# Kernel tuning notes

Hardware: AMD Instinct MI355X
Metric: run time of the kernel (lower is better)

## Reference

```python
import jax, jax.numpy as jnp
import numpy as np

B, N, D = 8, 8192, 64          # batch, input points, point feature dim
NPOINT, NSAMPLE = 1024, 16     # FPS samples S, KNN neighbors K
WN, OUT = 16, 128              # weightnet out channels, output channels
CIN = 3 + D                    # concat(xyz_norm, point feats) = linear in_channel
NEG_SLOPE = 0.1


def setup_inputs() -> dict:
    key = jax.random.key(0)
    ks = jax.random.split(key, 8)
    rn = lambda k, shp, s: jax.random.normal(k, shp, jnp.float32) * s
    return {
        "xyz": rn(ks[0], (B, 3, N), 1.0),
        "points": rn(ks[1], (B, D, N), 1.0),
        "w1": rn(ks[2], (3, 8), 0.5), "b1": jnp.zeros((8,), jnp.float32),
        "w2": rn(ks[3], (8, 8), 0.35), "b2": jnp.zeros((8,), jnp.float32),
        "w3": rn(ks[4], (8, WN), 0.35), "b3": jnp.zeros((WN,), jnp.float32),
        "lin_w": rn(ks[5], (WN * CIN, OUT), 0.03),
        "lin_b": jnp.zeros((OUT,), jnp.float32),
    }


def _fps(xyz):
    """Furthest point sampling. xyz: [B,N,3] -> idx [B,NPOINT] int32."""
    def step(carry, _):
        dist, farthest = carry  # [B,N], [B]
        centroid = jnp.take_along_axis(xyz, farthest[:, None, None], axis=1)  # [B,1,3]
        d = jnp.sum((xyz - centroid) ** 2, axis=-1)  # [B,N]
        dist = jnp.minimum(dist, d)
        return (dist, jnp.argmax(dist, axis=-1).astype(jnp.int32)), farthest
    init = (jnp.full((xyz.shape[0], xyz.shape[1]), 1e10, xyz.dtype),
            jnp.zeros((xyz.shape[0],), jnp.int32))
    _, idxs = jax.lax.scan(step, init, None, length=NPOINT)
    return idxs.T  # [B, NPOINT]


def reference(xyz, points, w1, b1, w2, b2, w3, b3, lin_w, lin_b):
    xyz_t = xyz.transpose(0, 2, 1)       # [B,N,3]
    pts_t = points.transpose(0, 2, 1)    # [B,N,D]

    fps_idx = _fps(xyz_t)                                   # [B,S]
    bidx = jnp.arange(B)[:, None]
    new_xyz = xyz_t[bidx, fps_idx]                          # [B,S,3]

    # KNN: squared distances (same ordering as euclidean cdist)
    sqr = jnp.sum((new_xyz[:, :, None, :] - xyz_t[:, None, :, :]) ** 2, axis=-1)  # [B,S,N]
    _, knn = jax.lax.top_k(-sqr, NSAMPLE)                   # [B,S,K]

    b3i = jnp.arange(B)[:, None, None]
    g_xyz = xyz_t[b3i, knn]                                 # [B,S,K,3]
    g_xyz_norm = g_xyz - new_xyz[:, :, None, :]             # [B,S,K,3]
    g_pts = pts_t[b3i, knn]                                 # [B,S,K,D]
    feat = jnp.concatenate([g_xyz_norm, g_pts], axis=-1)    # [B,S,K,3+D]

    # WeightNet: 1x1 convs == per-neighbor MLP on xyz offsets
    h = jax.nn.relu(g_xyz_norm @ w1 + b1)
    h = jax.nn.relu(h @ w2 + b2)
    wts = jax.nn.relu(h @ w3 + b3)                          # [B,S,K,WN]

    # weighted aggregation over K, then flatten [C, WN]
    agg = jnp.einsum('bskc,bskw->bscw', feat, wts).reshape(B, NPOINT, CIN * WN)
    out = agg @ lin_w + lin_b                               # [B,S,OUT]
    out = jnp.where(out > 0, out, NEG_SLOPE * out)          # LeakyReLU(0.1)

    return new_xyz.transpose(0, 2, 1), out.transpose(0, 2, 1), fps_idx
```

## Files before the change

### kernel.cpp

```cpp
#include <hip/hip_runtime.h>
#include <hip/hip_bf16.h>

#define NPTS   8192
#define NBATCH 8
#define S      1024
#define K      16
#define D      64
#define CIN    67
#define WN     16
#define OUTC   128

#define OUT_MAIN 24576
#define OUT_FPS  1073152

#define T_FPS   0
#define T_TP    8
#define T_WK    1032
#define NBLK    1544

#define SCOPE __HIP_MEMORY_SCOPE_AGENT

typedef float v2f __attribute__((ext_vector_type(2)));

struct Ctrl {
  int ticket;
  int pad0[31];
  int tp_done[8];
  int pad1[24];
  int prog[8];
};

__device__ __forceinline__ unsigned long long aload64(const unsigned long long* p) {
  return __hip_atomic_load(p, __ATOMIC_RELAXED, SCOPE);
}
__device__ __forceinline__ void astore64(unsigned long long* p, unsigned long long v) {
  __hip_atomic_store(p, v, __ATOMIC_RELAXED, SCOPE);
}

__device__ __forceinline__ void barrier_lgkm() {
  asm volatile("s_waitcnt lgkmcnt(0)\n\ts_barrier" ::: "memory");
}

template <int CTRL, int RM>
__device__ __forceinline__ unsigned long long dpp_max_step(unsigned long long key) {
  int lo = __builtin_amdgcn_update_dpp(0, (int)(unsigned)(key & 0xFFFFFFFFull), CTRL, RM, 0xF, true);
  int hi = __builtin_amdgcn_update_dpp(0, (int)(unsigned)(key >> 32),           CTRL, RM, 0xF, true);
  unsigned long long o = ((unsigned long long)(unsigned)hi << 32) | (unsigned)lo;
  return o > key ? o : key;
}

__device__ void fps_role(int b, const float* __restrict__ xyz,
                         unsigned long long* __restrict__ nxA,
                         unsigned long long* __restrict__ nxB,
                         float* __restrict__ out, Ctrl* ctrl, void* smem)
{
#pragma clang fp contract(off)
  float* s_x = (float*)smem;
  float* s_y = s_x + NPTS;
  float* s_z = s_y + NPTS;
  float4* hist = (float4*)((char*)smem + 98304);
  unsigned long long* slots = (unsigned long long*)((char*)smem + 114688);

  const int tid  = threadIdx.x;
  const int wave = tid >> 6;
  const int lane = tid & 63;
  const float* xb = xyz + (size_t)b * 3 * NPTS;

  v2f px[8], py[8], pz[8], dist[8];
#pragma unroll
  for (int p = 0; p < 8; p++) {
    int ne = (2 * p) * 512 + tid;
    int no = ne + 512;
    px[p] = (v2f){xb[ne], xb[no]};
    py[p] = (v2f){xb[NPTS + ne], xb[NPTS + no]};
    pz[p] = (v2f){xb[2 * NPTS + ne], xb[2 * NPTS + no]};
    dist[p] = (v2f){1e10f, 1e10f};
    s_x[ne] = px[p].x; s_x[no] = px[p].y;
    s_y[ne] = py[p].x; s_y[no] = py[p].y;
    s_z[ne] = pz[p].x; s_z[no] = pz[p].y;
  }

  int far = 0;
  float cx = xb[0], cy = xb[NPTS], cz = xb[2 * NPTS];

  for (int t = 0; t < 1024; t++) {
    if (tid == (t & 511))
      hist[t] = make_float4(cx, cy, cz, (float)far);

    if ((t & 31) == 0 && t > 0 && wave == 0 && lane < 32) {
      int tt = t - 32 + lane;
      float4 h = hist[tt];
      int gidx = (b << 10) + tt;
      astore64(&nxA[gidx],
               ((unsigned long long)__float_as_uint(h.x) << 32) | __float_as_uint(h.y));
      astore64(&nxB[gidx],
               ((unsigned long long)__float_as_uint(h.z) << 32) | (unsigned)((int)h.w + 1));
      if (lane == 0)
        __hip_atomic_store(&ctrl->prog[b], t, __ATOMIC_RELAXED, SCOPE);
    }

    const v2f c2x = (v2f){cx, cx}, c2y = (v2f){cy, cy}, c2z = (v2f){cz, cz};

    float bd_e = -1.0f, bd_o = -1.0f;
    int   ce   = 0,     co   = 0;
#pragma unroll
    for (int p = 0; p < 8; p++) {
      v2f dx = px[p] - c2x, dy = py[p] - c2y, dz = pz[p] - c2z;
      v2f d  = (dx * dx + dy * dy) + dz * dz;
      float nde = fminf(dist[p].x, d.x);
      float ndo = fminf(dist[p].y, d.y);
      dist[p].x = nde;
      dist[p].y = ndo;
      if (nde > bd_e) { bd_e = nde; ce = 2 * p; }
      if (ndo > bd_o) { bd_o = ndo; co = 2 * p + 1; }
    }

    unsigned long long ke =
        ((unsigned long long)__float_as_uint(bd_e) << 32) | (unsigned)(~(unsigned)(ce * 512 + tid));
    unsigned long long ko =
        ((unsigned long long)__float_as_uint(bd_o) << 32) | (unsigned)(~(unsigned)(co * 512 + tid));
    unsigned long long key = ko > ke ? ko : ke;

    key = dpp_max_step<0x111, 0xF>(key);
    key = dpp_max_step<0x112, 0xF>(key);
    key = dpp_max_step<0x114, 0xF>(key);
    key = dpp_max_step<0x118, 0xF>(key);
    key = dpp_max_step<0x142, 0xA>(key);
    key = dpp_max_step<0x143, 0xC>(key);
    if (lane == 63) slots[(t & 1) * 8 + wave] = key;
    barrier_lgkm();

    const unsigned long long* sl = slots + (t & 1) * 8;
    unsigned long long k0 = sl[0], k1 = sl[1], k2 = sl[2], k3 = sl[3];
    unsigned long long k4 = sl[4], k5 = sl[5], k6 = sl[6], k7 = sl[7];
    k0 = k1 > k0 ? k1 : k0;
    k2 = k3 > k2 ? k3 : k2;
    k4 = k5 > k4 ? k5 : k4;
    k6 = k7 > k6 ? k7 : k6;
    k0 = k2 > k0 ? k2 : k0;
    k4 = k6 > k4 ? k6 : k4;
    k0 = k4 > k0 ? k4 : k0;
    int gi = (int)(~(unsigned)(k0 & 0xFFFFFFFFull));
    far = gi;
    cx = s_x[gi]; cy = s_y[gi]; cz = s_z[gi];
  }
  __syncthreads();

  if (wave == 0 && lane < 32) {
    int tt = 992 + lane;
    float4 h = hist[tt];
    int gidx = (b << 10) + tt;
    astore64(&nxA[gidx],
             ((unsigned long long)__float_as_uint(h.x) << 32) | __float_as_uint(h.y));
    astore64(&nxB[gidx],
             ((unsigned long long)__float_as_uint(h.z) << 32) | (unsigned)((int)h.w + 1));
    if (lane == 0)
      __hip_atomic_store(&ctrl->prog[b], 1024, __ATOMIC_RELAXED, SCOPE);
  }

#pragma unroll
  for (int j = 0; j < 2; j++) {
    int t = j * 512 + tid;
    float4 h = hist[t];
    out[OUT_FPS + b * 1024 + t] = h.w;
    out[b * 3072 + t]           = h.x;
    out[b * 3072 + 1024 + t]    = h.y;
    out[b * 3072 + 2048 + t]    = h.z;
  }
}

__device__ void tp_role(int bid, const float* __restrict__ pts, float* __restrict__ ptt,
                        Ctrl* ctrl, void* smem)
{
  float* tile = (float*)smem;
  const int b  = bid >> 7;
  const int n0 = (bid & 127) * 64;
  const float* pb = pts + (size_t)b * D * NPTS;
#pragma unroll
  for (int i = 0; i < 8; i++) {
    int s = threadIdx.x + i * 512;
    int nl = s & 63, d = s >> 6;
    tile[d * 65 + nl] = pb[(size_t)d * NPTS + n0 + nl];
  }
  __syncthreads();
  float* ob = ptt + ((size_t)b * NPTS + n0) * D;
#pragma unroll
  for (int i = 0; i < 8; i++) {
    int s = threadIdx.x + i * 512;
    int dl = s & 63, nl = s >> 6;
    ob[(size_t)nl * D + dl] = tile[dl * 65 + nl];
  }
  __syncthreads();
  if (threadIdx.x == 0)
    __hip_atomic_fetch_add(&ctrl->tp_done[b], 1, __ATOMIC_RELEASE, SCOPE);
}

__device__ void worker_role(int u, const float* __restrict__ xyz,
                            const unsigned long long* __restrict__ nxA,
                            const unsigned long long* __restrict__ nxB,
                            const float* __restrict__ ptt,
                            const float* __restrict__ w1, const float* __restrict__ b1,
                            const float* __restrict__ w2, const float* __restrict__ b2,
                            const float* __restrict__ w3, const float* __restrict__ b3,
                            const float* __restrict__ lin_w, const float* __restrict__ lin_b,
                            float* __restrict__ agg, float* __restrict__ out,
                            Ctrl* ctrl, void* smem)
{
  const int tid = threadIdx.x;
  const int b   = u & 7;
  const int q   = u >> 3;
  const int c0  = q * 16;
  const int cbase = (b << 10) + c0;

  unsigned long long* s_k = (unsigned long long*)smem;
  float* s_cc = (float*)((char*)smem + 69760);
  int*   s_nk = (int*)((char*)smem + 70016);

  if (tid == 0) {
    const int need = c0 + 16;
    int p;
    while ((p = __hip_atomic_load(&ctrl->prog[b], __ATOMIC_RELAXED, SCOPE)) < need) {
      if (need - p > 64) __builtin_amdgcn_s_sleep(127);
      else               __builtin_amdgcn_s_sleep(16);
    }
  }
  __syncthreads();

  if (tid < 16) {
    unsigned long long Bv, Av;
    while ((unsigned)((Bv = aload64(&nxB[cbase + tid])) & 0xFFFFFFFFull) == 0u)
      __builtin_amdgcn_s_sleep(2);
    while ((Av = aload64(&nxA[cbase + tid])) == 0ull)
      __builtin_amdgcn_s_sleep(1);
    s_cc[tid * 4 + 0] = __uint_as_float((unsigned)(Av >> 32));
    s_cc[tid * 4 + 1] = __uint_as_float((unsigned)(Av & 0xFFFFFFFFull));
    s_cc[tid * 4 + 2] = __uint_as_float((unsigned)(Bv >> 32));
  }
  __syncthreads();

  {
#pragma clang fp contract(off)
    const int cl    = tid >> 5;
    const int chunk = tid & 31;
    const float* xb = xyz + (size_t)b * 3 * NPTS;
    const float cx = s_cc[cl * 4 + 0];
    const float cy = s_cc[cl * 4 + 1];
    const float cz = s_cc[cl * 4 + 2];

    float nd[16]; int ni[16];
#pragma unroll
    for (int k = 0; k < 16; k++) { nd[k] = 3.4e38f; ni[k] = 0x7FFFFFFF; }

    for (int jj = 0; jj < 256; jj++) {
      int j = jj * 32 + chunk;
      float dx = xb[j] - cx, dy = xb[NPTS + j] - cy, dz = xb[2 * NPTS + j] - cz;
      float d  = (dx * dx + dy * dy) + dz * dz;
      float cv = d; int iv = j;
#pragma unroll
      for (int k = 0; k < 16; k++) {
        bool sw = cv < nd[k];
        float tv = nd[k]; int ti = ni[k];
        nd[k] = sw ? cv : tv;  ni[k] = sw ? iv : ti;
        cv    = sw ? tv : cv;  iv    = sw ? ti : iv;
      }
    }
#pragma unroll
    for (int k = 0; k < 16; k++)
      s_k[cl * 545 + chunk * 17 + k] =
          ((unsigned long long)__float_as_uint(nd[k]) << 32) | (unsigned)ni[k];
    s_k[cl * 545 + chunk * 17 + 16] = ~0ull;
  }
  __syncthreads();

  if (tid < 16) {
    int pos[32];
#pragma unroll
    for (int c = 0; c < 32; c++) pos[c] = 0;
    for (int r = 0; r < 16; r++) {
      unsigned long long bk = ~0ull; int bc = 0;
#pragma unroll
      for (int c = 0; c < 32; c++) {
        unsigned long long kv = s_k[tid * 545 + c * 17 + pos[c]];
        if (kv < bk) { bk = kv; bc = c; }
      }
#pragma unroll
      for (int c = 0; c < 32; c++) pos[c] += (c == bc);
      s_nk[tid * 16 + r] = (int)(bk & 0xFFFFFFFFull);
    }
  }
  if (tid == 0)
    while (__hip_atomic_load(&ctrl->tp_done[b], __ATOMIC_RELAXED, SCOPE) < 128)
      __builtin_amdgcn_s_sleep(8);
  __syncthreads();

  float* s_wts = (float*)smem;
  float* s_off = s_wts + 8 * 272;
  const int wv   = tid >> 6;
  const int lane = tid & 63;

  for (int it = 0; it < 2; it++) {
    const int cl2  = it * 8 + wv;
    const int csel = cbase + cl2;
    if (lane < 16) {
      int nk = s_nk[cl2 * 16 + lane];
      const float* xb = xyz + (size_t)b * 3 * NPTS;
      float ox = xb[nk]            - s_cc[cl2 * 4 + 0];
      float oy = xb[NPTS + nk]     - s_cc[cl2 * 4 + 1];
      float oz = xb[2 * NPTS + nk] - s_cc[cl2 * 4 + 2];
      s_off[wv * 48 + lane * 3 + 0] = ox;
      s_off[wv * 48 + lane * 3 + 1] = oy;
      s_off[wv * 48 + lane * 3 + 2] = oz;
      float h1[8], h2[8];
#pragma unroll
      for (int j = 0; j < 8; j++)
        h1[j] = fmaxf(0.f, ox * w1[j] + oy * w1[8 + j] + oz * w1[16 + j] + b1[j]);
#pragma unroll
      for (int j = 0; j < 8; j++) {
        float a = b2[j];
#pragma unroll
        for (int i = 0; i < 8; i++) a = fmaf(h1[i], w2[i * 8 + j], a);
        h2[j] = fmaxf(0.f, a);
      }
#pragma unroll
      for (int w = 0; w < 16; w++) {
        float a = b3[w];
#pragma unroll
        for (int i = 0; i < 8; i++) a = fmaf(h2[i], w3[i * 16 + w], a);
        s_wts[wv * 272 + lane * 17 + w] = fmaxf(0.f, a);
      }
    }
    __syncthreads();

    float f[16];
#pragma unroll
    for (int k = 0; k < 16; k++) {
      int nk = s_nk[cl2 * 16 + k];
      f[k] = ptt[((size_t)b * NPTS + nk) * D + lane];
    }
    float acc[16];
#pragma unroll
    for (int w = 0; w < 16; w++) acc[w] = 0.f;
#pragma unroll
    for (int k = 0; k < 16; k++) {
#pragma unroll
      for (int w = 0; w < 16; w++)
        acc[w] = fmaf(f[k], s_wts[wv * 272 + k * 17 + w], acc[w]);
    }
    float* arow = agg + (size_t)csel * (CIN * WN) + (3 + lane) * 16;
#pragma unroll
    for (int qq = 0; qq < 4; qq++) {
      float4 v = make_float4(acc[4 * qq], acc[4 * qq + 1], acc[4 * qq + 2], acc[4 * qq + 3]);
      *(float4*)(arow + 4 * qq) = v;
    }
    if (lane < 48) {
      int c = lane >> 4, w = lane & 15;
      float a = 0.f;
#pragma unroll
      for (int k = 0; k < 16; k++)
        a = fmaf(s_off[wv * 48 + k * 3 + c], s_wts[wv * 272 + k * 17 + w], a);
      agg[(size_t)csel * (CIN * WN) + c * 16 + w] = a;
    }
    __syncthreads();
  }

  float* a_t = (float*)smem;
  float* b_t = a_t + 16 * 17;
  float acc2[2][2] = {};
  for (int kt = 0; kt < 67; kt++) {
    const int k0 = kt * 16;
    if (tid < 256) {
      int r = tid & 15, kk = tid >> 4;
      a_t[kk * 17 + r] = agg[(size_t)(cbase + r) * (CIN * WN) + k0 + kk];
    }
#pragma unroll
    for (int i = 0; i < 4; i++) {
      int idx = tid + i * 512;
      int c = idx & 127, kk = idx >> 7;
      b_t[kk * 128 + c] = lin_w[(size_t)(k0 + kk) * OUTC + c];
    }
    __syncthreads();
#pragma unroll
    for (int kk = 0; kk < 16; kk++) {
      float a0 = a_t[kk * 17 + wv * 2];
      float a1 = a_t[kk * 17 + wv * 2 + 1];
      float bv0 = b_t[kk * 128 + lane * 2];
      float bv1 = b_t[kk * 128 + lane * 2 + 1];
      acc2[0][0] = fmaf(a0, bv0, acc2[0][0]);
      acc2[0][1] = fmaf(a0, bv1, acc2[0][1]);
      acc2[1][0] = fmaf(a1, bv0, acc2[1][0]);
      acc2[1][1] = fmaf(a1, bv1, acc2[1][1]);
    }
    __syncthreads();
  }
#pragma unroll
  for (int j = 0; j < 2; j++) {
#pragma unroll
    for (int cc = 0; cc < 2; cc++) {
      int ss = c0 + wv * 2 + j;
      int C  = lane * 2 + cc;
      float v = acc2[j][cc] + lin_b[C];
      v = v > 0.f ? v : 0.1f * v;
      out[OUT_MAIN + ((size_t)(b * OUTC + C)) * 1024 + ss] = v;
    }
  }
}

__global__ __launch_bounds__(512)
void mega_kernel(const float* __restrict__ xyz, const float* __restrict__ pts,
                 const float* __restrict__ w1, const float* __restrict__ b1,
                 const float* __restrict__ w2, const float* __restrict__ b2,
                 const float* __restrict__ w3, const float* __restrict__ b3,
                 const float* __restrict__ lin_w, const float* __restrict__ lin_b,
                 float* __restrict__ out, unsigned long long* __restrict__ nxA,
                 unsigned long long* __restrict__ nxB,
                 float* __restrict__ ptt, float* __restrict__ agg, Ctrl* ctrl)
{
  __shared__ __align__(16) unsigned long long smem[14400];
  __shared__ int s_ticket;
  if (threadIdx.x == 0)
    s_ticket = __hip_atomic_fetch_add(&ctrl->ticket, 1, __ATOMIC_RELAXED, SCOPE);
  __syncthreads();
  const int tk = s_ticket;

  if (tk < T_TP)
    fps_role(tk, xyz, nxA, nxB, out, ctrl, smem);
  else if (tk < T_WK)
    tp_role(tk - T_TP, pts, ptt, ctrl, smem);
  else
    worker_role(tk - T_WK, xyz, nxA, nxB, ptt, w1, b1, w2, b2, w3, b3,
                lin_w, lin_b, agg, out, ctrl, smem);
}

extern "C" void kernel_launch(void* const* d_in, const int* in_sizes, int n_in,
                              void* d_out, int out_size, void* d_ws, size_t ws_size,
                              hipStream_t stream) {
  const float* xyz    = (const float*)d_in[0];
  const float* points = (const float*)d_in[1];
  const float* w1     = (const float*)d_in[2];
  const float* b1     = (const float*)d_in[3];
  const float* w2     = (const float*)d_in[4];
  const float* b2     = (const float*)d_in[5];
  const float* w3     = (const float*)d_in[6];
  const float* b3     = (const float*)d_in[7];
  const float* lin_w  = (const float*)d_in[8];
  const float* lin_b  = (const float*)d_in[9];
  float* out = (float*)d_out;
  char*  ws  = (char*)d_ws;

  Ctrl* ctrl              = (Ctrl*)(ws);
  unsigned long long* nxA = (unsigned long long*)(ws + 4096);
  unsigned long long* nxB = (unsigned long long*)(ws + 69632);
  float* ptt              = (float*)(ws + 1048576);
  float* agg              = (float*)(ws + 17825792);

  hipMemsetAsync(ws, 0, 135168, stream);
  mega_kernel<<<NBLK, 512, 0, stream>>>(xyz, points, w1, b1, w2, b2, w3, b3,
                                        lin_w, lin_b, out, nxA, nxB, ptt, agg, ctrl);
}
```

Before: 1.278 ms.

## Spatially bucket points for FPS and prune buckets via bounding-box distance bounds

Rewrites the furthest-point-sampling role so points are sorted into 512 spatial grid cells and packed into 128 buckets of 64 points, each with a bounding box. Every iteration only buckets whose box lower bound can still beat their current max distance are re-evaluated, and a DPP reduction over the per-bucket keys picks the winner. This targets the serial FPS critical path by skipping distance updates for far buckets. In exchange it adds extra barriers, LDS atomics and list building per step, and raises the shared memory footprint for every block, which may cut occupancy for the worker blocks.

```diff
diff --git a/kernel.cpp b/kernel.cpp
--- a/kernel.cpp
+++ b/kernel.cpp
@@ -20,8 +20,6 @@
 
 #define SCOPE __HIP_MEMORY_SCOPE_AGENT
 
-typedef float v2f __attribute__((ext_vector_type(2)));
-
 struct Ctrl {
   int ticket;
   int pad0[31];
@@ -42,11 +40,12 @@
 }
 
 template <int CTRL, int RM>
-__device__ __forceinline__ unsigned long long dpp_max_step(unsigned long long key) {
+__device__ __forceinline__ void dpp_max_pair(unsigned long long& key, int& pos) {
   int lo = __builtin_amdgcn_update_dpp(0, (int)(unsigned)(key & 0xFFFFFFFFull), CTRL, RM, 0xF, true);
   int hi = __builtin_amdgcn_update_dpp(0, (int)(unsigned)(key >> 32),           CTRL, RM, 0xF, true);
+  int op = __builtin_amdgcn_update_dpp(0, pos,                                  CTRL, RM, 0xF, true);
   unsigned long long o = ((unsigned long long)(unsigned)hi << 32) | (unsigned)lo;
-  return o > key ? o : key;
+  if (o > key) { key = o; pos = op; }
 }
 
 __device__ void fps_role(int b, const float* __restrict__ xyz,
@@ -55,42 +54,118 @@
                          float* __restrict__ out, Ctrl* ctrl, void* smem)
 {
 #pragma clang fp contract(off)
-  float* s_x = (float*)smem;
-  float* s_y = s_x + NPTS;
-  float* s_z = s_y + NPTS;
-  float4* hist = (float4*)((char*)smem + 98304);
-  unsigned long long* slots = (unsigned long long*)((char*)smem + 114688);
+  char* bp = (char*)smem;
+  float4*             sp4   = (float4*)bp;
+  unsigned short*     sidx  = (unsigned short*)(bp + 131072);
+  float*              bbox  = (float*)(bp + 147456);
+  unsigned long long* bkey  = (unsigned long long*)(bp + 150528);
+  int*                bpos  = (int*)(bp + 151552);
+  int*                dlist = (int*)(bp + 152064);
+  int*                cnt   = (int*)(bp + 152576);
+  unsigned long long* skey  = (unsigned long long*)(bp + 152592);
+  int*                sposl = (int*)(bp + 152608);
+  float4*             ring  = (float4*)(bp + 152624);
+  int* hist = (int*)(bp + 147456);
+  int* offs = (int*)(bp + 149504);
 
   const int tid  = threadIdx.x;
   const int wave = tid >> 6;
   const int lane = tid & 63;
   const float* xb = xyz + (size_t)b * 3 * NPTS;
 
-  v2f px[8], py[8], pz[8], dist[8];
-#pragma unroll
-  for (int p = 0; p < 8; p++) {
-    int ne = (2 * p) * 512 + tid;
-    int no = ne + 512;
-    px[p] = (v2f){xb[ne], xb[no]};
-    py[p] = (v2f){xb[NPTS + ne], xb[NPTS + no]};
-    pz[p] = (v2f){xb[2 * NPTS + ne], xb[2 * NPTS + no]};
-    dist[p] = (v2f){1e10f, 1e10f};
-    s_x[ne] = px[p].x; s_x[no] = px[p].y;
-    s_y[ne] = py[p].x; s_y[no] = py[p].y;
-    s_z[ne] = pz[p].x; s_z[no] = pz[p].y;
-  }
+  float px[16], py[16], pz[16];
+  int   cid[16];
+#pragma unroll
+  for (int i = 0; i < 16; i++) {
+    int n = i * 512 + tid;
+    px[i] = xb[n]; py[i] = xb[NPTS + n]; pz[i] = xb[2 * NPTS + n];
+  }
+  float mnx = px[0], mxx = px[0], mny = py[0], mxy = py[0], mnz = pz[0], mxz = pz[0];
+#pragma unroll
+  for (int i = 1; i < 16; i++) {
+    mnx = fminf(mnx, px[i]); mxx = fmaxf(mxx, px[i]);
+    mny = fminf(mny, py[i]); mxy = fmaxf(mxy, py[i]);
+    mnz = fminf(mnz, pz[i]); mxz = fmaxf(mxz, pz[i]);
+  }
+#pragma unroll
+  for (int off = 1; off < 64; off <<= 1) {
+    mnx = fminf(mnx, __shfl_xor(mnx, off)); mxx = fmaxf(mxx, __shfl_xor(mxx, off));
+    mny = fminf(mny, __shfl_xor(mny, off)); mxy = fmaxf(mxy, __shfl_xor(mxy, off));
+    mnz = fminf(mnz, __shfl_xor(mnz, off)); mxz = fmaxf(mxz, __shfl_xor(mxz, off));
+  }
+  if (lane == 0) {
+    ring[wave]     = make_float4(mnx, mxx, mny, mxy);
+    ring[8 + wave] = make_float4(mnz, mxz, 0.f, 0.f);
+  }
+  if (tid < 512) hist[tid] = 0;
+  __syncthreads();
+  float LX = ring[0].x, HX = ring[0].y, LY = ring[0].z, HY = ring[0].w;
+  float LZ = ring[8].x, HZ = ring[8].y;
+#pragma unroll
+  for (int w = 1; w < 8; w++) {
+    LX = fminf(LX, ring[w].x); HX = fmaxf(HX, ring[w].y);
+    LY = fminf(LY, ring[w].z); HY = fmaxf(HY, ring[w].w);
+    LZ = fminf(LZ, ring[8 + w].x); HZ = fmaxf(HZ, ring[8 + w].y);
+  }
+  const float sx = 7.999f / fmaxf(HX - LX, 1e-30f);
+  const float sy = 7.999f / fmaxf(HY - LY, 1e-30f);
+  const float sz = 7.999f / fmaxf(HZ - LZ, 1e-30f);
+#pragma unroll
+  for (int i = 0; i < 16; i++) {
+    int ix = min(7, max(0, (int)((px[i] - LX) * sx)));
+    int iy = min(7, max(0, (int)((py[i] - LY) * sy)));
+    int iz = min(7, max(0, (int)((pz[i] - LZ) * sz)));
+    cid[i] = (iz << 6) | (iy << 3) | ix;
+    atomicAdd(&hist[cid[i]], 1);
+  }
+  __syncthreads();
+  if (tid < 512) {
+    int s = 0;
+    for (int k = 0; k < tid; k++) s += hist[k];
+    offs[tid] = s;
+  }
+  __syncthreads();
+#pragma unroll
+  for (int i = 0; i < 16; i++) {
+    int slot = atomicAdd(&offs[cid[i]], 1);
+    sp4[slot]  = make_float4(px[i], py[i], pz[i], 1e10f);
+    sidx[slot] = (unsigned short)(i * 512 + tid);
+  }
+  __syncthreads();
+  if (tid < 128) {
+    float lx = 3.4e38f, hx = -3.4e38f, ly = 3.4e38f, hy = -3.4e38f, lz = 3.4e38f, hz = -3.4e38f;
+    for (int m = 0; m < 64; m++) {
+      float4 P = sp4[tid * 64 + m];
+      lx = fminf(lx, P.x); hx = fmaxf(hx, P.x);
+      ly = fminf(ly, P.y); hy = fmaxf(hy, P.y);
+      lz = fminf(lz, P.z); hz = fmaxf(hz, P.z);
+    }
+    bbox[tid * 6 + 0] = lx; bbox[tid * 6 + 1] = hx;
+    bbox[tid * 6 + 2] = ly; bbox[tid * 6 + 3] = hy;
+    bbox[tid * 6 + 4] = lz; bbox[tid * 6 + 5] = hz;
+    bkey[tid] = (unsigned long long)0x7F7FFFFFu << 32;
+    bpos[tid] = 0;
+  }
+  if (tid == 0) cnt[0] = 0;
+  __syncthreads();
 
   int far = 0;
   float cx = xb[0], cy = xb[NPTS], cz = xb[2 * NPTS];
 
   for (int t = 0; t < 1024; t++) {
-    if (tid == (t & 511))
-      hist[t] = make_float4(cx, cy, cz, (float)far);
-
+    const int parity = t & 1;
+    if (tid == (t & 511)) {
+      ring[t & 63] = make_float4(cx, cy, cz, (float)far);
+      cnt[parity ^ 1] = 0;
+    }
     if ((t & 31) == 0 && t > 0 && wave == 0 && lane < 32) {
       int tt = t - 32 + lane;
-      float4 h = hist[tt];
+      float4 h = ring[tt & 63];
       int gidx = (b << 10) + tt;
+      out[OUT_FPS + b * 1024 + tt] = h.w;
+      out[b * 3072 + tt]           = h.x;
+      out[b * 3072 + 1024 + tt]    = h.y;
+      out[b * 3072 + 2048 + tt]    = h.z;
       astore64(&nxA[gidx],
                ((unsigned long long)__float_as_uint(h.x) << 32) | __float_as_uint(h.y));
       astore64(&nxB[gidx],
@@ -99,73 +174,86 @@
         __hip_atomic_store(&ctrl->prog[b], t, __ATOMIC_RELAXED, SCOPE);
     }
 
-    const v2f c2x = (v2f){cx, cx}, c2y = (v2f){cy, cy}, c2z = (v2f){cz, cz};
-
-    float bd_e = -1.0f, bd_o = -1.0f;
-    int   ce   = 0,     co   = 0;
-#pragma unroll
-    for (int p = 0; p < 8; p++) {
-      v2f dx = px[p] - c2x, dy = py[p] - c2y, dz = pz[p] - c2z;
-      v2f d  = (dx * dx + dy * dy) + dz * dz;
-      float nde = fminf(dist[p].x, d.x);
-      float ndo = fminf(dist[p].y, d.y);
-      dist[p].x = nde;
-      dist[p].y = ndo;
-      if (nde > bd_e) { bd_e = nde; ce = 2 * p; }
-      if (ndo > bd_o) { bd_o = ndo; co = 2 * p + 1; }
-    }
-
-    unsigned long long ke =
-        ((unsigned long long)__float_as_uint(bd_e) << 32) | (unsigned)(~(unsigned)(ce * 512 + tid));
-    unsigned long long ko =
-        ((unsigned long long)__float_as_uint(bd_o) << 32) | (unsigned)(~(unsigned)(co * 512 + tid));
-    unsigned long long key = ko > ke ? ko : ke;
-
-    key = dpp_max_step<0x111, 0xF>(key);
-    key = dpp_max_step<0x112, 0xF>(key);
-    key = dpp_max_step<0x114, 0xF>(key);
-    key = dpp_max_step<0x118, 0xF>(key);
-    key = dpp_max_step<0x142, 0xA>(key);
-    key = dpp_max_step<0x143, 0xC>(key);
-    if (lane == 63) slots[(t & 1) * 8 + wave] = key;
+    if (tid < 128) {
+      float maxd = __uint_as_float((unsigned)(bkey[tid] >> 32));
+      float ux = fmaxf(0.f, fmaxf(bbox[tid * 6 + 0] - cx, cx - bbox[tid * 6 + 1]));
+      float uy = fmaxf(0.f, fmaxf(bbox[tid * 6 + 2] - cy, cy - bbox[tid * 6 + 3]));
+      float uz = fmaxf(0.f, fmaxf(bbox[tid * 6 + 4] - cz, cz - bbox[tid * 6 + 5]));
+      float lb = (ux * ux + uy * uy) + uz * uz;
+      if (lb * 0.999999f < maxd) {
+        int s = atomicAdd(&cnt[parity], 1);
+        dlist[s] = tid;
+      }
+    }
     barrier_lgkm();
 
-    const unsigned long long* sl = slots + (t & 1) * 8;
-    unsigned long long k0 = sl[0], k1 = sl[1], k2 = sl[2], k3 = sl[3];
-    unsigned long long k4 = sl[4], k5 = sl[5], k6 = sl[6], k7 = sl[7];
-    k0 = k1 > k0 ? k1 : k0;
-    k2 = k3 > k2 ? k3 : k2;
-    k4 = k5 > k4 ? k5 : k4;
-    k6 = k7 > k6 ? k7 : k6;
-    k0 = k2 > k0 ? k2 : k0;
-    k4 = k6 > k4 ? k6 : k4;
-    k0 = k4 > k0 ? k4 : k0;
-    int gi = (int)(~(unsigned)(k0 & 0xFFFFFFFFull));
-    far = gi;
-    cx = s_x[gi]; cy = s_y[gi]; cz = s_z[gi];
+    const int Dn = cnt[parity];
+    for (int p = 0; p * 64 < Dn; p++) {
+      int g = p * 64 + (tid >> 3);
+      if (g < Dn) {
+        int j = dlist[g];
+        int base = j * 64 + (tid & 7) * 8;
+        uint4 iw = *(const uint4*)(sidx + base);
+        unsigned long long gk = 0; int gp = 0;
+#pragma unroll
+        for (int m = 0; m < 8; m++) {
+          float4 P = sp4[base + m];
+          float dx = P.x - cx, dy = P.y - cy, dz = P.z - cz;
+          float d  = (dx * dx + dy * dy) + dz * dz;
+          float nd = fminf(P.w, d);
+          ((float*)&sp4[base + m])[3] = nd;
+          unsigned oi = (((const unsigned*)&iw)[m >> 1] >> ((m & 1) * 16)) & 0xFFFFu;
+          unsigned long long key =
+              ((unsigned long long)__float_as_uint(nd) << 32) | (unsigned)(~oi);
+          if (key > gk) { gk = key; gp = base + m; }
+        }
+#pragma unroll
+        for (int w = 1; w < 8; w <<= 1) {
+          unsigned long long ok = __shfl_xor(gk, w, 8);
+          int op = __shfl_xor(gp, w, 8);
+          if (ok > gk) { gk = ok; gp = op; }
+        }
+        if ((tid & 7) == 0) { bkey[j] = gk; bpos[j] = gp; }
+      }
+    }
+    barrier_lgkm();
+
+    if (wave == 0) {
+      unsigned long long k1 = bkey[lane], k2 = bkey[64 + lane];
+      int p1 = bpos[lane], p2 = bpos[64 + lane];
+      if (k2 > k1) { k1 = k2; p1 = p2; }
+      dpp_max_pair<0x111, 0xF>(k1, p1);
+      dpp_max_pair<0x112, 0xF>(k1, p1);
+      dpp_max_pair<0x114, 0xF>(k1, p1);
+      dpp_max_pair<0x118, 0xF>(k1, p1);
+      dpp_max_pair<0x142, 0xA>(k1, p1);
+      dpp_max_pair<0x143, 0xC>(k1, p1);
+      if (lane == 63) { skey[parity] = k1; sposl[parity] = p1; }
+    }
+    barrier_lgkm();
+
+    unsigned long long KW = skey[parity];
+    int PW = sposl[parity];
+    far = (int)(~(unsigned)(KW & 0xFFFFFFFFull));
+    float4 c4 = sp4[PW];
+    cx = c4.x; cy = c4.y; cz = c4.z;
   }
   __syncthreads();
 
   if (wave == 0 && lane < 32) {
     int tt = 992 + lane;
-    float4 h = hist[tt];
+    float4 h = ring[tt & 63];
     int gidx = (b << 10) + tt;
+    out[OUT_FPS + b * 1024 + tt] = h.w;
+    out[b * 3072 + tt]           = h.x;
+    out[b * 3072 + 1024 + tt]    = h.y;
+    out[b * 3072 + 2048 + tt]    = h.z;
     astore64(&nxA[gidx],
              ((unsigned long long)__float_as_uint(h.x) << 32) | __float_as_uint(h.y));
     astore64(&nxB[gidx],
              ((unsigned long long)__float_as_uint(h.z) << 32) | (unsigned)((int)h.w + 1));
     if (lane == 0)
       __hip_atomic_store(&ctrl->prog[b], 1024, __ATOMIC_RELAXED, SCOPE);
-  }
-
-#pragma unroll
-  for (int j = 0; j < 2; j++) {
-    int t = j * 512 + tid;
-    float4 h = hist[t];
-    out[OUT_FPS + b * 1024 + t] = h.w;
-    out[b * 3072 + t]           = h.x;
-    out[b * 3072 + 1024 + t]    = h.y;
-    out[b * 3072 + 2048 + t]    = h.z;
   }
 }
 
@@ -415,7 +503,7 @@
                  unsigned long long* __restrict__ nxB,
                  float* __restrict__ ptt, float* __restrict__ agg, Ctrl* ctrl)
 {
-  __shared__ __align__(16) unsigned long long smem[14400];
+  __shared__ __align__(16) unsigned long long smem[19232];
   __shared__ int s_ticket;
   if (threadIdx.x == 0)
     s_ticket = __hip_atomic_fetch_add(&ctrl->ticket, 1, __ATOMIC_RELAXED, SCOPE);
```

Result: slower. 1.987 ms (+55.4%).
